# Performance work log

Measured on AMD Instinct MI355X. Metric: run time of the kernel, lower is better.

## Reference

```python
import jax, jax.numpy as jnp
import numpy as np

VOCAB = 50257
D_MODEL = 1024
LN_EPS = 1e-5


def setup_inputs() -> dict:
    key = jax.random.key(0)
    k1, k2, k3, k4 = jax.random.split(key, 4)
    enc_out = jax.random.normal(k1, (2, 2048, D_MODEL), dtype=jnp.float32)
    # posterior_proj: Linear(d_model, vocab) -> weight [vocab, d_model], bias [vocab]
    scale = 1.0 / np.sqrt(D_MODEL)
    proj_w = jax.random.uniform(k2, (VOCAB, D_MODEL), jnp.float32, -scale, scale)
    proj_b = jax.random.uniform(k3, (VOCAB,), jnp.float32, -scale, scale)
    # vocab_embedding.weight [vocab, d_model]
    emb = jax.random.normal(k4, (VOCAB, D_MODEL), dtype=jnp.float32)
    ln_gamma = jnp.ones((D_MODEL,), jnp.float32)
    ln_beta = jnp.zeros((D_MODEL,), jnp.float32)
    return {"enc_out": enc_out, "proj_w": proj_w, "proj_b": proj_b,
            "emb": emb, "ln_gamma": ln_gamma, "ln_beta": ln_beta}


def _layer_norm(x, gamma, beta):
    mu = jnp.mean(x, axis=-1, keepdims=True)
    var = jnp.mean(jnp.square(x - mu), axis=-1, keepdims=True)
    return (x - mu) * jax.lax.rsqrt(var + LN_EPS) * gamma + beta


def reference(enc_out, proj_w, proj_b, emb, ln_gamma, ln_beta):
    # logits: [B, S, V]
    logits = jnp.einsum('bsd,vd->bsv', enc_out, proj_w) + proj_b
    probs = jax.nn.softmax(logits, axis=-1)
    # soft vocab lookup: [B, S, D]
    soft_emb = jnp.einsum('bsv,vd->bsd', probs, emb)
    return _layer_norm(enc_out + soft_emb, ln_gamma, ln_beta)
```

## Files before the change

### kernel.cpp

```cpp
#include <hip/hip_runtime.h>
#include <hip/hip_bf16.h>
#include <stdint.h>

#define D_MODEL 1024
#define VOCAB 50257
#define VP 51200
#define ROWS 4096
#define LN_EPS 1e-5f

typedef short s16x8 __attribute__((ext_vector_type(8)));
typedef float f32x4 __attribute__((ext_vector_type(4)));

__device__ __forceinline__ unsigned short f2bf(float f) {
  union { __hip_bfloat16 h; unsigned short u; } cv;
  cv.h = __float2bfloat16(f);
  return cv.u;
}
__device__ __forceinline__ void gload_lds16(const void* g, void* l) {
  __builtin_amdgcn_global_load_lds(
      (const __attribute__((address_space(1))) unsigned int*)g,
      (__attribute__((address_space(3))) unsigned int*)l, 16, 0, 0);
}

__global__ __launch_bounds__(256) void k_cast_enc(const float* __restrict__ src,
                                                  unsigned short* __restrict__ dst) {
  const size_t i0 = ((size_t)blockIdx.x * 256 + threadIdx.x) * 8;
  const f32x4* p = reinterpret_cast<const f32x4*>(src + i0);
  f32x4 a = p[0], b = p[1];
  s16x8 o;
  o[0]=f2bf(a[0]); o[1]=f2bf(a[1]); o[2]=f2bf(a[2]); o[3]=f2bf(a[3]);
  o[4]=f2bf(b[0]); o[5]=f2bf(b[1]); o[6]=f2bf(b[2]); o[7]=f2bf(b[3]);
  *reinterpret_cast<s16x8*>(dst + i0) = o;
}

__global__ __launch_bounds__(256) void k_pack_wlin(const float* __restrict__ src,
                                                   unsigned short* __restrict__ dst) {
  const size_t i0 = ((size_t)blockIdx.x * 256 + threadIdx.x) * 8;
  const int v = (int)(i0 >> 10);
  s16x8 o;
  if (v < VOCAB) {
    const f32x4* p = reinterpret_cast<const f32x4*>(src + i0);
    f32x4 a = p[0], b = p[1];
    o[0]=f2bf(a[0]); o[1]=f2bf(a[1]); o[2]=f2bf(a[2]); o[3]=f2bf(a[3]);
    o[4]=f2bf(b[0]); o[5]=f2bf(b[1]); o[6]=f2bf(b[2]); o[7]=f2bf(b[3]);
  } else {
    #pragma unroll
    for (int i = 0; i < 8; ++i) o[i] = 0;
  }
  *reinterpret_cast<s16x8*>(dst + i0) = o;
}

__global__ __launch_bounds__(256) void k_pack_et(const float* __restrict__ emb,
                                                 unsigned short* __restrict__ et) {
  __shared__ float tile[32][33];
  const int v0 = blockIdx.x * 32;
  const int d0 = blockIdx.y * 32;
  const int tx = threadIdx.x, ty = threadIdx.y;
  #pragma unroll
  for (int i = 0; i < 4; ++i) {
    const int v = v0 + ty + 8 * i;
    tile[ty + 8 * i][tx] = (v < VOCAB) ? emb[(size_t)v * D_MODEL + d0 + tx] : 0.f;
  }
  __syncthreads();
  #pragma unroll
  for (int i = 0; i < 4; ++i) {
    const int d = d0 + ty + 8 * i;
    et[(size_t)d * VP + v0 + tx] = f2bf(tile[tx][ty + 8 * i]);
  }
}

__global__ __launch_bounds__(512, 4)
void k_gemm1(const unsigned short* __restrict__ encb,
             const unsigned short* __restrict__ Wb,
             const float* __restrict__ bias,
             unsigned short* __restrict__ P,
             float* __restrict__ den) {
  __shared__ __align__(16) unsigned short As[128 * 64];
  __shared__ __align__(16) unsigned short Bs[256 * 64];

  const int bx = blockIdx.x;
  const int xcd = bx & 7, bi = bx >> 3;
  const int mt_ = bi & 31;
  const int nt_ = xcd * 25 + (bi >> 5);
  const int row0 = mt_ * 128;
  const int col0 = nt_ * 256;

  const int tid = threadIdx.x;
  const int w = tid >> 6, l = tid & 63;
  const int mw = w >> 2, nw = w & 3;
  const int r16 = l & 15, g = l >> 4;

  f32x4 acc[4][4];
  #pragma unroll
  for (int a = 0; a < 4; ++a)
    #pragma unroll
    for (int b = 0; b < 4; ++b) acc[a][b] = f32x4{0.f, 0.f, 0.f, 0.f};

  uint32_t arow[4], asw[4], brow[4], bsw[4];
  #pragma unroll
  for (int t = 0; t < 4; ++t) {
    const uint32_t ar = mw * 64 + t * 16 + r16;
    arow[t] = ar * 128; asw[t] = (ar & 7) << 4;
    const uint32_t br = nw * 64 + t * 16 + r16;
    brow[t] = br * 128; bsw[t] = (br & 7) << 4;
  }

  for (int kt = 0; kt < 16; ++kt) {
    __syncthreads();
    #pragma unroll
    for (int ii = 0; ii < 2; ++ii) {
      const int c = tid + ii * 512;
      const int r = c >> 3, s2 = (c & 7) ^ (r & 7);
      gload_lds16(encb + (size_t)(row0 + r) * 1024 + kt * 64 + s2 * 8, &As[c * 8]);
    }
    #pragma unroll
    for (int ii = 0; ii < 4; ++ii) {
      const int c = tid + ii * 512;
      const int r = c >> 3, s2 = (c & 7) ^ (r & 7);
      gload_lds16(Wb + (size_t)(col0 + r) * 1024 + kt * 64 + s2 * 8, &Bs[c * 8]);
    }
    __syncthreads();

    #pragma unroll
    for (int kk = 0; kk < 2; ++kk) {
      const uint32_t ksl = (uint32_t)((kk * 4 + g) << 4);
      s16x8 af[4], bf[4];
      #pragma unroll
      for (int t = 0; t < 4; ++t) {
        af[t] = *reinterpret_cast<const s16x8*>(
            reinterpret_cast<const char*>(As) + arow[t] + (ksl ^ asw[t]));
        bf[t] = *reinterpret_cast<const s16x8*>(
            reinterpret_cast<const char*>(Bs) + brow[t] + (ksl ^ bsw[t]));
      }
      #pragma unroll
      for (int a = 0; a < 4; ++a)
        #pragma unroll
        for (int b = 0; b < 4; ++b)
          acc[a][b] = __builtin_amdgcn_mfma_f32_16x16x32_bf16(af[a], bf[b], acc[a][b], 0, 0, 0);
    }
  }

  float biasv[4];
  #pragma unroll
  for (int b = 0; b < 4; ++b) {
    const int v = col0 + nw * 64 + b * 16 + r16;
    biasv[b] = (v < VOCAB) ? bias[v] : 0.f;
  }
  #pragma unroll
  for (int a = 0; a < 4; ++a) {
    #pragma unroll
    for (int j = 0; j < 4; ++j) {
      const int q = row0 + mw * 64 + a * 16 + g * 4 + j;
      float rsum = 0.f;
      #pragma unroll
      for (int b = 0; b < 4; ++b) {
        const int v = col0 + nw * 64 + b * 16 + r16;
        float e = (v < VOCAB) ? __expf(acc[a][b][j] + biasv[b]) : 0.f;
        rsum += e;
        P[(size_t)q * VP + v] = f2bf(e);
      }
      rsum += __shfl_xor(rsum, 1);
      rsum += __shfl_xor(rsum, 2);
      rsum += __shfl_xor(rsum, 4);
      rsum += __shfl_xor(rsum, 8);
      if (r16 == 0) atomicAdd(&den[(size_t)q * 8 + (nt_ & 7)], rsum);
    }
  }
}

__global__ __launch_bounds__(512, 4)
void k_gemm2(const unsigned short* __restrict__ P,
             const unsigned short* __restrict__ ET,
             float* __restrict__ opart) {
  __shared__ __align__(16) unsigned short As[256 * 64];
  __shared__ __align__(16) unsigned short Bs[128 * 64];

  const int bx = blockIdx.x;
  const int ks = bx & 7, bi = bx >> 3;
  const int nd = bi & 7, mt_ = bi >> 3;
  const int row0 = mt_ * 256, col0 = nd * 128;
  const int k0 = ks * (VP / 8);

  const int tid = threadIdx.x;
  const int w = tid >> 6, l = tid & 63;
  const int mw = w >> 1, nw = w & 1;
  const int r16 = l & 15, g = l >> 4;

  f32x4 acc[4][4];
  #pragma unroll
  for (int a = 0; a < 4; ++a)
    #pragma unroll
    for (int b = 0; b < 4; ++b) acc[a][b] = f32x4{0.f, 0.f, 0.f, 0.f};

  uint32_t arow[4], asw[4], brow[4], bsw[4];
  #pragma unroll
  for (int t = 0; t < 4; ++t) {
    const uint32_t ar = mw * 64 + t * 16 + r16;
    arow[t] = ar * 128; asw[t] = (ar & 7) << 4;
    const uint32_t br = nw * 64 + t * 16 + r16;
    brow[t] = br * 128; bsw[t] = (br & 7) << 4;
  }

  for (int kt = 0; kt < 100; ++kt) {
    const int koff = k0 + kt * 64;
    __syncthreads();
    #pragma unroll
    for (int ii = 0; ii < 4; ++ii) {
      const int c = tid + ii * 512;
      const int r = c >> 3, s2 = (c & 7) ^ (r & 7);
      gload_lds16(P + (size_t)(row0 + r) * VP + koff + s2 * 8, &As[c * 8]);
    }
    #pragma unroll
    for (int ii = 0; ii < 2; ++ii) {
      const int c = tid + ii * 512;
      const int r = c >> 3, s2 = (c & 7) ^ (r & 7);
      gload_lds16(ET + (size_t)(col0 + r) * VP + koff + s2 * 8, &Bs[c * 8]);
    }
    __syncthreads();

    #pragma unroll
    for (int kk = 0; kk < 2; ++kk) {
      const uint32_t ksl = (uint32_t)((kk * 4 + g) << 4);
      s16x8 af[4], bf[4];
      #pragma unroll
      for (int t = 0; t < 4; ++t) {
        af[t] = *reinterpret_cast<const s16x8*>(
            reinterpret_cast<const char*>(As) + arow[t] + (ksl ^ asw[t]));
        bf[t] = *reinterpret_cast<const s16x8*>(
            reinterpret_cast<const char*>(Bs) + brow[t] + (ksl ^ bsw[t]));
      }
      #pragma unroll
      for (int a = 0; a < 4; ++a)
        #pragma unroll
        for (int b = 0; b < 4; ++b)
          acc[a][b] = __builtin_amdgcn_mfma_f32_16x16x32_bf16(af[a], bf[b], acc[a][b], 0, 0, 0);
    }
  }

  #pragma unroll
  for (int a = 0; a < 4; ++a) {
    #pragma unroll
    for (int j = 0; j < 4; ++j) {
      const int q = row0 + mw * 64 + a * 16 + g * 4 + j;
      float* orow = opart + ((size_t)ks * ROWS + q) * D_MODEL;
      #pragma unroll
      for (int b = 0; b < 4; ++b) {
        const int d = col0 + nw * 64 + b * 16 + r16;
        orow[d] = acc[a][b][j];
      }
    }
  }
}

__global__ __launch_bounds__(256)
void k_ln2(const float* __restrict__ enc, const float* __restrict__ opart,
           const float* __restrict__ den, const float* __restrict__ gam,
           const float* __restrict__ bet, float* __restrict__ out) {
  __shared__ float r1[4], r2[4];
  const int row = blockIdx.x;
  const int t = threadIdx.x;
  const int d = t * 4;
  float dn = 0.f;
  #pragma unroll
  for (int s = 0; s < 8; ++s) dn += den[(size_t)row * 8 + s];
  const float inv = 1.f / dn;
  f32x4 acc = {0.f, 0.f, 0.f, 0.f};
  #pragma unroll
  for (int ks = 0; ks < 8; ++ks) {
    const f32x4 a = *reinterpret_cast<const f32x4*>(opart + ((size_t)ks * ROWS + row) * D_MODEL + d);
    #pragma unroll
    for (int jj = 0; jj < 4; ++jj) acc[jj] += a[jj];
  }
  const f32x4 e = *reinterpret_cast<const f32x4*>(enc + (size_t)row * D_MODEL + d);
  f32x4 y;
  #pragma unroll
  for (int jj = 0; jj < 4; ++jj) y[jj] = e[jj] + acc[jj] * inv;
  float s1 = y[0] + y[1] + y[2] + y[3];
  float s2 = y[0]*y[0] + y[1]*y[1] + y[2]*y[2] + y[3]*y[3];
  #pragma unroll
  for (int off = 1; off < 64; off <<= 1) {
    s1 += __shfl_xor(s1, off);
    s2 += __shfl_xor(s2, off);
  }
  if ((t & 63) == 0) { r1[t >> 6] = s1; r2[t >> 6] = s2; }
  __syncthreads();
  const float S1 = r1[0] + r1[1] + r1[2] + r1[3];
  const float S2 = r2[0] + r2[1] + r2[2] + r2[3];
  const float mean = S1 * (1.f / D_MODEL);
  const float var = S2 * (1.f / D_MODEL) - mean * mean;
  const float rs = rsqrtf(var + LN_EPS);
  const f32x4 gv = *reinterpret_cast<const f32x4*>(gam + d);
  const f32x4 bv = *reinterpret_cast<const f32x4*>(bet + d);
  f32x4 o;
  #pragma unroll
  for (int jj = 0; jj < 4; ++jj) o[jj] = (y[jj] - mean) * rs * gv[jj] + bv[jj];
  *reinterpret_cast<f32x4*>(out + (size_t)row * D_MODEL + d) = o;
}

extern "C" void kernel_launch(void* const* d_in, const int* in_sizes, int n_in,
                              void* d_out, int out_size, void* d_ws, size_t ws_size,
                              hipStream_t stream) {
  const float* enc = (const float*)d_in[0];
  const float* pw  = (const float*)d_in[1];
  const float* pb  = (const float*)d_in[2];
  const float* emb = (const float*)d_in[3];
  const float* gam = (const float*)d_in[4];
  const float* bet = (const float*)d_in[5];
  float* out = (float*)d_out;

  size_t off = 0;
  unsigned short* encb = (unsigned short*)((char*)d_ws + off); off += (size_t)ROWS * D_MODEL * 2;
  unsigned short* Wb   = (unsigned short*)((char*)d_ws + off); off += (size_t)VP * D_MODEL * 2;
  unsigned short* ET   = (unsigned short*)((char*)d_ws + off); off += (size_t)D_MODEL * VP * 2;
  unsigned short* P    = (unsigned short*)((char*)d_ws + off); off += (size_t)ROWS * VP * 2;
  float* opart         = (float*)((char*)d_ws + off);          off += (size_t)8 * ROWS * D_MODEL * 4;
  float* den           = (float*)((char*)d_ws + off);          off += (size_t)ROWS * 8 * 4;

  if (off > ws_size) {
    hipMemsetAsync(d_out, 0x7f, (size_t)out_size * 4, stream);
    return;
  }

  hipMemsetAsync(den, 0, (size_t)ROWS * 8 * 4, stream);
  k_cast_enc<<<(ROWS * D_MODEL / 8) / 256, 256, 0, stream>>>(enc, encb);
  k_pack_wlin<<<((size_t)VP * D_MODEL / 8) / 256, 256, 0, stream>>>(pw, Wb);
  k_pack_et<<<dim3(VP / 32, D_MODEL / 32), dim3(32, 8), 0, stream>>>(emb, ET);
  k_gemm1<<<6400, 512, 0, stream>>>(encb, Wb, pb, P, den);
  k_gemm2<<<1024, 512, 0, stream>>>(P, ET, opart);
  k_ln2<<<ROWS, 256, 0, stream>>>(enc, opart, den, gam, bet, out);
}
```

Measured before the change: 1.162 ms.

## Triple-buffer LDS stages with split async prefetch in both GEMM kernels

Both GEMM main loops now keep three LDS stages and prefetch the tile two iterations ahead. The prefetch is split into two halves interleaved with the two MFMA sub-steps, and the per-iteration pair of __syncthreads is replaced by one explicit vmcnt wait plus a barrier. MFMA sections are bracketed with s_setprio so they get issue priority. The aim is to hide global-to-LDS load latency behind compute. In exchange, the larger LDS footprint drops occupancy from 4 to 2 blocks per CU.

```diff
diff --git a/kernel.cpp b/kernel.cpp
--- a/kernel.cpp
+++ b/kernel.cpp
@@ -69,14 +69,14 @@
   }
 }
 
-__global__ __launch_bounds__(512, 4)
+__global__ __launch_bounds__(512, 2)
 void k_gemm1(const unsigned short* __restrict__ encb,
              const unsigned short* __restrict__ Wb,
              const float* __restrict__ bias,
              unsigned short* __restrict__ P,
              float* __restrict__ den) {
-  __shared__ __align__(16) unsigned short As[128 * 64];
-  __shared__ __align__(16) unsigned short Bs[256 * 64];
+  __shared__ __align__(16) unsigned short As[3][128 * 64];
+  __shared__ __align__(16) unsigned short Bs[3][256 * 64];
 
   const int bx = blockIdx.x;
   const int xcd = bx & 7, bi = bx >> 3;
@@ -90,6 +90,16 @@
   const int mw = w >> 2, nw = w & 3;
   const int r16 = l & 15, g = l >> 4;
 
+  const int cA = tid;
+  const int rA0 = cA >> 3,        sA0 = ((cA & 7) ^ (rA0 & 7)) * 8;
+  const int rA1 = (cA + 512) >> 3, sA1 = (((cA + 512) & 7) ^ (rA1 & 7)) * 8;
+  const int rB0 = cA >> 3,        sB0 = sA0;
+  const int rB1 = rA1,            sB1 = sA1;
+  const int rB2 = (cA + 1024) >> 3, sB2 = (((cA + 1024) & 7) ^ (rB2 & 7)) * 8;
+  const int rB3 = (cA + 1536) >> 3, sB3 = (((cA + 1536) & 7) ^ (rB3 & 7)) * 8;
+  const unsigned short* gA = encb + (size_t)row0 * 1024;
+  const unsigned short* gB = Wb + (size_t)col0 * 1024;
+
   f32x4 acc[4][4];
   #pragma unroll
   for (int a = 0; a < 4; ++a)
@@ -105,40 +115,64 @@
     brow[t] = br * 128; bsw[t] = (br & 7) << 4;
   }
 
+#define G1_STAGE_P1(kt_, s_)                                                   \
+  do {                                                                         \
+    const int ko = (kt_) * 64;                                                 \
+    gload_lds16(gA + (size_t)rA0 * 1024 + ko + sA0, &As[s_][cA * 8]);          \
+    gload_lds16(gA + (size_t)rA1 * 1024 + ko + sA1, &As[s_][(cA + 512) * 8]);  \
+    gload_lds16(gB + (size_t)rB0 * 1024 + ko + sB0, &Bs[s_][cA * 8]);          \
+    gload_lds16(gB + (size_t)rB1 * 1024 + ko + sB1, &Bs[s_][(cA + 512) * 8]);  \
+  } while (0)
+#define G1_STAGE_P2(kt_, s_)                                                   \
+  do {                                                                         \
+    const int ko = (kt_) * 64;                                                 \
+    gload_lds16(gB + (size_t)rB2 * 1024 + ko + sB2, &Bs[s_][(cA + 1024) * 8]); \
+    gload_lds16(gB + (size_t)rB3 * 1024 + ko + sB3, &Bs[s_][(cA + 1536) * 8]); \
+  } while (0)
+
+  G1_STAGE_P1(0, 0); G1_STAGE_P2(0, 0);
+  G1_STAGE_P1(1, 1); G1_STAGE_P2(1, 1);
+  asm volatile("s_waitcnt vmcnt(6)" ::: "memory");
+  __builtin_amdgcn_sched_barrier(0);
+  __builtin_amdgcn_s_barrier();
+  __builtin_amdgcn_sched_barrier(0);
+
+  int s = 0;
   for (int kt = 0; kt < 16; ++kt) {
-    __syncthreads();
-    #pragma unroll
-    for (int ii = 0; ii < 2; ++ii) {
-      const int c = tid + ii * 512;
-      const int r = c >> 3, s2 = (c & 7) ^ (r & 7);
-      gload_lds16(encb + (size_t)(row0 + r) * 1024 + kt * 64 + s2 * 8, &As[c * 8]);
-    }
-    #pragma unroll
-    for (int ii = 0; ii < 4; ++ii) {
-      const int c = tid + ii * 512;
-      const int r = c >> 3, s2 = (c & 7) ^ (r & 7);
-      gload_lds16(Wb + (size_t)(col0 + r) * 1024 + kt * 64 + s2 * 8, &Bs[c * 8]);
-    }
-    __syncthreads();
-
+    const int sn = (s == 2) ? 0 : s + 1;
+    const int sn2 = (sn == 2) ? 0 : sn + 1;
+    const char* Ab = reinterpret_cast<const char*>(As[s]);
+    const char* Bb = reinterpret_cast<const char*>(Bs[s]);
     #pragma unroll
     for (int kk = 0; kk < 2; ++kk) {
+      if (kk == 0) { if (kt + 2 < 16) G1_STAGE_P1(kt + 2, sn2); }
+      else         { if (kt + 2 < 16) G1_STAGE_P2(kt + 2, sn2); }
       const uint32_t ksl = (uint32_t)((kk * 4 + g) << 4);
       s16x8 af[4], bf[4];
       #pragma unroll
       for (int t = 0; t < 4; ++t) {
-        af[t] = *reinterpret_cast<const s16x8*>(
-            reinterpret_cast<const char*>(As) + arow[t] + (ksl ^ asw[t]));
-        bf[t] = *reinterpret_cast<const s16x8*>(
-            reinterpret_cast<const char*>(Bs) + brow[t] + (ksl ^ bsw[t]));
+        af[t] = *reinterpret_cast<const s16x8*>(Ab + arow[t] + (ksl ^ asw[t]));
+        bf[t] = *reinterpret_cast<const s16x8*>(Bb + brow[t] + (ksl ^ bsw[t]));
       }
+      __builtin_amdgcn_s_setprio(1);
       #pragma unroll
       for (int a = 0; a < 4; ++a)
         #pragma unroll
         for (int b = 0; b < 4; ++b)
           acc[a][b] = __builtin_amdgcn_mfma_f32_16x16x32_bf16(af[a], bf[b], acc[a][b], 0, 0, 0);
-    }
-  }
+      __builtin_amdgcn_s_setprio(0);
+    }
+    if (kt < 15) {
+      if (kt + 2 < 16) asm volatile("s_waitcnt vmcnt(6)" ::: "memory");
+      else             asm volatile("s_waitcnt vmcnt(0)" ::: "memory");
+      __builtin_amdgcn_sched_barrier(0);
+      __builtin_amdgcn_s_barrier();
+      __builtin_amdgcn_sched_barrier(0);
+    }
+    s = sn;
+  }
+#undef G1_STAGE_P1
+#undef G1_STAGE_P2
 
   float biasv[4];
   #pragma unroll
@@ -168,12 +202,12 @@
   }
 }
 
-__global__ __launch_bounds__(512, 4)
+__global__ __launch_bounds__(512, 2)
 void k_gemm2(const unsigned short* __restrict__ P,
              const unsigned short* __restrict__ ET,
              float* __restrict__ opart) {
-  __shared__ __align__(16) unsigned short As[256 * 64];
-  __shared__ __align__(16) unsigned short Bs[128 * 64];
+  __shared__ __align__(16) unsigned short As[3][256 * 64];
+  __shared__ __align__(16) unsigned short Bs[3][128 * 64];
 
   const int bx = blockIdx.x;
   const int ks = bx & 7, bi = bx >> 3;
@@ -186,6 +220,14 @@
   const int mw = w >> 1, nw = w & 1;
   const int r16 = l & 15, g = l >> 4;
 
+  const int cA = tid;
+  const int rA0 = cA >> 3,          sA0 = ((cA & 7) ^ (rA0 & 7)) * 8;
+  const int rA1 = (cA + 512) >> 3,  sA1 = (((cA + 512) & 7) ^ (rA1 & 7)) * 8;
+  const int rA2 = (cA + 1024) >> 3, sA2 = (((cA + 1024) & 7) ^ (rA2 & 7)) * 8;
+  const int rA3 = (cA + 1536) >> 3, sA3 = (((cA + 1536) & 7) ^ (rA3 & 7)) * 8;
+  const unsigned short* gA = P + (size_t)row0 * VP + k0;
+  const unsigned short* gB = ET + (size_t)col0 * VP + k0;
+
   f32x4 acc[4][4];
   #pragma unroll
   for (int a = 0; a < 4; ++a)
@@ -201,41 +243,64 @@
     brow[t] = br * 128; bsw[t] = (br & 7) << 4;
   }
 
+#define G2_STAGE_P1(kt_, s_)                                                   \
+  do {                                                                         \
+    const int ko = (kt_) * 64;                                                 \
+    gload_lds16(gA + (size_t)rA0 * VP + ko + sA0, &As[s_][cA * 8]);            \
+    gload_lds16(gA + (size_t)rA1 * VP + ko + sA1, &As[s_][(cA + 512) * 8]);    \
+    gload_lds16(gA + (size_t)rA2 * VP + ko + sA2, &As[s_][(cA + 1024) * 8]);   \
+    gload_lds16(gA + (size_t)rA3 * VP + ko + sA3, &As[s_][(cA + 1536) * 8]);   \
+  } while (0)
+#define G2_STAGE_P2(kt_, s_)                                                   \
+  do {                                                                         \
+    const int ko = (kt_) * 64;                                                 \
+    gload_lds16(gB + (size_t)rA0 * VP + ko + sA0, &Bs[s_][cA * 8]);            \
+    gload_lds16(gB + (size_t)rA1 * VP + ko + sA1, &Bs[s_][(cA + 512) * 8]);    \
+  } while (0)
+
+  G2_STAGE_P1(0, 0); G2_STAGE_P2(0, 0);
+  G2_STAGE_P1(1, 1); G2_STAGE_P2(1, 1);
+  asm volatile("s_waitcnt vmcnt(6)" ::: "memory");
+  __builtin_amdgcn_sched_barrier(0);
+  __builtin_amdgcn_s_barrier();
+  __builtin_amdgcn_sched_barrier(0);
+
+  int s = 0;
   for (int kt = 0; kt < 100; ++kt) {
-    const int koff = k0 + kt * 64;
-    __syncthreads();
-    #pragma unroll
-    for (int ii = 0; ii < 4; ++ii) {
-      const int c = tid + ii * 512;
-      const int r = c >> 3, s2 = (c & 7) ^ (r & 7);
-      gload_lds16(P + (size_t)(row0 + r) * VP + koff + s2 * 8, &As[c * 8]);
-    }
-    #pragma unroll
-    for (int ii = 0; ii < 2; ++ii) {
-      const int c = tid + ii * 512;
-      const int r = c >> 3, s2 = (c & 7) ^ (r & 7);
-      gload_lds16(ET + (size_t)(col0 + r) * VP + koff + s2 * 8, &Bs[c * 8]);
-    }
-    __syncthreads();
-
+    const int sn = (s == 2) ? 0 : s + 1;
+    const int sn2 = (sn == 2) ? 0 : sn + 1;
+    const char* Ab = reinterpret_cast<const char*>(As[s]);
+    const char* Bb = reinterpret_cast<const char*>(Bs[s]);
     #pragma unroll
     for (int kk = 0; kk < 2; ++kk) {
+      if (kk == 0) { if (kt + 2 < 100) G2_STAGE_P1(kt + 2, sn2); }
+      else         { if (kt + 2 < 100) G2_STAGE_P2(kt + 2, sn2); }
       const uint32_t ksl = (uint32_t)((kk * 4 + g) << 4);
       s16x8 af[4], bf[4];
       #pragma unroll
       for (int t = 0; t < 4; ++t) {
-        af[t] = *reinterpret_cast<const s16x8*>(
-            reinterpret_cast<const char*>(As) + arow[t] + (ksl ^ asw[t]));
-        bf[t] = *reinterpret_cast<const s16x8*>(
-            reinterpret_cast<const char*>(Bs) + brow[t] + (ksl ^ bsw[t]));
+        af[t] = *reinterpret_cast<const s16x8*>(Ab + arow[t] + (ksl ^ asw[t]));
+        bf[t] = *reinterpret_cast<const s16x8*>(Bb + brow[t] + (ksl ^ bsw[t]));
       }
+      __builtin_amdgcn_s_setprio(1);
       #pragma unroll
       for (int a = 0; a < 4; ++a)
         #pragma unroll
         for (int b = 0; b < 4; ++b)
           acc[a][b] = __builtin_amdgcn_mfma_f32_16x16x32_bf16(af[a], bf[b], acc[a][b], 0, 0, 0);
-    }
-  }
+      __builtin_amdgcn_s_setprio(0);
+    }
+    if (kt < 99) {
+      if (kt + 2 < 100) asm volatile("s_waitcnt vmcnt(6)" ::: "memory");
+      else              asm volatile("s_waitcnt vmcnt(0)" ::: "memory");
+      __builtin_amdgcn_sched_barrier(0);
+      __builtin_amdgcn_s_barrier();
+      __builtin_amdgcn_sched_barrier(0);
+    }
+    s = sn;
+  }
+#undef G2_STAGE_P1
+#undef G2_STAGE_P2
 
   #pragma unroll
   for (int a = 0; a < 4; ++a) {
```

After: 1.918 ms. +65.1%, slower.
